# Kernel optimization log

Hardware: AMD Instinct MI355X
Metric: run time of the kernel (lower is better)

## Reference

```python
import jax, jax.numpy as jnp
import numpy as np

B, S, D, H, DFF = 8, 1024, 1024, 16, 4096
DK = D // H
EPS = 1e-6
NEG = -1e9


def setup_inputs() -> dict:
    key = jax.random.key(0)
    ks = jax.random.split(key, 8)
    x = jax.random.normal(ks[0], (B, S, D), dtype=jnp.float32)
    mask = jnp.ones((B, 1, 1, S), dtype=jnp.int32)
    s = 0.02
    wq = jax.random.normal(ks[1], (D, D), jnp.float32) * s
    wk = jax.random.normal(ks[2], (D, D), jnp.float32) * s
    wv = jax.random.normal(ks[3], (D, D), jnp.float32) * s
    wo = jax.random.normal(ks[4], (D, D), jnp.float32) * s
    bq = jnp.zeros((D,), jnp.float32); bk = jnp.zeros((D,), jnp.float32)
    bv = jnp.zeros((D,), jnp.float32); bo = jnp.zeros((D,), jnp.float32)
    w1 = jax.random.normal(ks[5], (D, DFF), jnp.float32) * s
    b1 = jnp.zeros((DFF,), jnp.float32)
    w2 = jax.random.normal(ks[6], (DFF, D), jnp.float32) * s
    b2 = jnp.zeros((D,), jnp.float32)
    g1 = jnp.array(1.0, jnp.float32); be1 = jnp.array(0.0, jnp.float32)
    g2 = jnp.array(1.0, jnp.float32); be2 = jnp.array(0.0, jnp.float32)
    return dict(x=x, mask=mask, wq=wq, bq=bq, wk=wk, bk=bk, wv=wv, bv=bv,
                wo=wo, bo=bo, w1=w1, b1=b1, w2=w2, b2=b2,
                g1=g1, be1=be1, g2=g2, be2=be2)


def layer_norm(x, gamma, beta):
    # repo quirk: unbiased std (ddof=1), scalar gamma/beta, divide by (std+eps)
    mean = jnp.mean(x, axis=-1, keepdims=True)
    std = jnp.std(x, axis=-1, keepdims=True, ddof=1)
    return gamma * (x - mean) / (std + EPS) + beta


def mha(x, mask, wq, bq, wk, bk, wv, bv, wo, bo):
    q = (x @ wq + bq).reshape(B, S, H, DK).transpose(0, 2, 1, 3)  # bhsd
    k = (x @ wk + bk).reshape(B, S, H, DK).transpose(0, 2, 1, 3)
    v = (x @ wv + bv).reshape(B, S, H, DK).transpose(0, 2, 1, 3)
    scores = jnp.einsum('bhqd,bhkd->bhqk', q, k) / jnp.sqrt(jnp.float32(DK))
    scores = jnp.where(mask == 0, NEG, scores)
    attn = jax.nn.softmax(scores, axis=-1)
    out = jnp.einsum('bhqk,bhkd->bhqd', attn, v)
    out = out.transpose(0, 2, 1, 3).reshape(B, S, D)
    return out @ wo + bo


def reference(x, mask, wq, bq, wk, bk, wv, bv, wo, bo, w1, b1, w2, b2, g1, be1, g2, be2):
    # pre-LN residual: x + sublayer(norm(x)); dropout inert at eval
    x = x + mha(layer_norm(x, g1, be1), mask, wq, bq, wk, bk, wv, bv, wo, bo)
    h = layer_norm(x, g2, be2)
    x = x + (jax.nn.relu(h @ w1 + b1) @ w2 + b2)
    return x
```

## Files before the change

### kernel.cpp

```cpp
#include <hip/hip_runtime.h>
#include <math.h>

typedef __bf16 bf16;
typedef float f32x4 __attribute__((ext_vector_type(4)));
typedef bf16 bf16x8 __attribute__((ext_vector_type(8)));
typedef bf16 bf16x4 __attribute__((ext_vector_type(4)));

#define DEV __device__ __forceinline__

constexpr int Ss = 1024, Dd = 1024;
constexpr float EPSf = 1e-6f;
constexpr float SM_SCALE = 0.125f * 1.4426950408889634f;

DEV void gl_lds16(const void* g, void* l) {
  __builtin_amdgcn_global_load_lds(
      (const __attribute__((address_space(1))) void*)g,
      (__attribute__((address_space(3))) void*)l, 16, 0, 0);
}

__global__ __launch_bounds__(256) void transpose6_k(
    const float* __restrict__ i0, const float* __restrict__ i1,
    const float* __restrict__ i2, const float* __restrict__ i3,
    const float* __restrict__ i4, const float* __restrict__ i5,
    bf16* __restrict__ o0, bf16* __restrict__ o1, bf16* __restrict__ o2,
    bf16* __restrict__ o3, bf16* __restrict__ o4, bf16* __restrict__ o5) {
  __shared__ float t[64 * 65];
  const int bi = blockIdx.x;
  const float* in;
  bf16* out;
  int R, C, local, sh;
  if (bi < 1024) {
    const int j = bi >> 8;
    local = bi & 255; R = 1024; C = 1024; sh = 4;
    in = (j == 0) ? i0 : (j == 1) ? i1 : (j == 2) ? i2 : i3;
    out = (j == 0) ? o0 : (j == 1) ? o1 : (j == 2) ? o2 : o3;
  } else if (bi < 2048) {
    local = bi - 1024; R = 1024; C = 4096; sh = 6; in = i4; out = o4;
  } else {
    local = bi - 2048; R = 4096; C = 1024; sh = 4; in = i5; out = o5;
  }
  const int nx = 1 << sh;
  const int bx = local & (nx - 1), by = local >> sh;
  const int tid = threadIdx.x;
  const int tx = tid & 63, ty = tid >> 6;
  const int r0 = by * 64, c0 = bx * 64;
#pragma unroll
  for (int i = 0; i < 16; i++) {
    int r = ty + i * 4;
    t[r * 65 + tx] = in[(size_t)(r0 + r) * C + c0 + tx];
  }
  __syncthreads();
#pragma unroll
  for (int i = 0; i < 16; i++) {
    int r = ty + i * 4;
    out[(size_t)(c0 + r) * R + r0 + tx] = (bf16)t[tx * 65 + r];
  }
}

__global__ __launch_bounds__(256) void ln_kernel(
    const float* __restrict__ in, bf16* __restrict__ out,
    const float* __restrict__ gp, const float* __restrict__ bp) {
  const int row = blockIdx.x;
  const int tid = threadIdx.x;
  float v[4];
  const float* p = in + (size_t)row * Dd + tid * 4;
#pragma unroll
  for (int i = 0; i < 4; i++) v[i] = p[i];
  float s = v[0] + v[1] + v[2] + v[3];
  float s2 = v[0] * v[0] + v[1] * v[1] + v[2] * v[2] + v[3] * v[3];
#pragma unroll
  for (int m = 1; m < 64; m <<= 1) {
    s += __shfl_xor(s, m, 64);
    s2 += __shfl_xor(s2, m, 64);
  }
  __shared__ float ls[4], ls2[4];
  if ((tid & 63) == 0) {
    ls[tid >> 6] = s;
    ls2[tid >> 6] = s2;
  }
  __syncthreads();
  s = ls[0] + ls[1] + ls[2] + ls[3];
  s2 = ls2[0] + ls2[1] + ls2[2] + ls2[3];
  float mean = s * (1.0f / Dd);
  float var = (s2 - (float)Dd * mean * mean) * (1.0f / (Dd - 1));
  var = fmaxf(var, 0.0f);
  float g = gp[0], be = bp[0];
  float rs = g / (sqrtf(var) + EPSf);
  bf16* q = out + (size_t)row * Dd + tid * 4;
#pragma unroll
  for (int i = 0; i < 4; i++) q[i] = (bf16)((v[i] - mean) * rs + be);
}

template <int EPI, int BK>
__global__ __launch_bounds__(256) void gemm_bt(
    const bf16* __restrict__ A, const bf16* __restrict__ Bt,
    const float* __restrict__ bias, const float* __restrict__ bias2,
    const float* __restrict__ bias3, const float* __restrict__ resid,
    bf16* __restrict__ vtb, void* __restrict__ Cout, int M, int N, int K,
    int sa, int sb) {
  __shared__ __attribute__((aligned(16))) char smem[2 * 128 * BK * 2];
  bf16* As = (bf16*)smem;
  bf16* Bs = (bf16*)(smem + 128 * BK * 2);
  constexpr int CPR = BK / 8;
  constexpr int RPJ = 256 / CPR;
  constexpr int NJ = BK / 16;
  const int tid = threadIdx.x;
  const int ln = tid & 63;
  const int wv = tid >> 6;
  const int wm = wv >> 1, wn = wv & 1;
  const int quad = ln >> 4, l16 = ln & 15;
  const int l7 = l16 & 7;
  const int m0 = blockIdx.y * 128, n0 = blockIdx.x * 128;

  f32x4 acc[4][4];
#pragma unroll
  for (int i = 0; i < 4; i++)
#pragma unroll
    for (int j = 0; j < 4; j++) acc[i][j] = {0.f, 0.f, 0.f, 0.f};

  const int sr = tid / CPR;
  const int sc = (tid & (CPR - 1)) ^ (sr & 7);
  const size_t abase = (size_t)(m0 + sr) * sa + sc * 8;
  const size_t bbase = (size_t)(n0 + sr) * sb + sc * 8;

  for (int k0 = 0; k0 < K; k0 += BK) {
#pragma unroll
    for (int j = 0; j < NJ; j++) {
      gl_lds16(A + abase + (size_t)(j * RPJ) * sa + k0,
               (char*)As + j * 4096 + wv * 1024);
      gl_lds16(Bt + bbase + (size_t)(j * RPJ) * sb + k0,
               (char*)Bs + j * 4096 + wv * 1024);
    }
    __syncthreads();
#pragma unroll
    for (int kh = 0; kh < BK / 32; kh++) {
      bf16x8 af[4], bfr[4];
#pragma unroll
      for (int mi = 0; mi < 4; mi++)
        af[mi] = *(const bf16x8*)&As[(wm * 64 + mi * 16 + l16) * BK +
                                     ((kh * 4 + quad) ^ l7) * 8];
#pragma unroll
      for (int ni = 0; ni < 4; ni++)
        bfr[ni] = *(const bf16x8*)&Bs[(wn * 64 + ni * 16 + l16) * BK +
                                      ((kh * 4 + quad) ^ l7) * 8];
#pragma unroll
      for (int mi = 0; mi < 4; mi++)
#pragma unroll
        for (int ni = 0; ni < 4; ni++)
          acc[mi][ni] = __builtin_amdgcn_mfma_f32_16x16x32_bf16(
              af[mi], bfr[ni], acc[mi][ni], 0, 0, 0);
    }
    __syncthreads();
  }

  if constexpr (EPI == 4) {
    if (n0 < 2048) {
#pragma unroll
      for (int mi = 0; mi < 4; mi++) {
        const int m = m0 + wm * 64 + mi * 16 + quad * 4;
#pragma unroll
        for (int ni = 0; ni < 4; ni++) {
          const int n = n0 + wn * 64 + ni * 16 + l16;
          const float bvl = (n < 1024) ? bias[n] : bias2[n - 1024];
#pragma unroll
          for (int r = 0; r < 4; r++)
            ((bf16*)Cout)[(size_t)(m + r) * N + n] =
                (bf16)(acc[mi][ni][r] + bvl);
        }
      }
    } else {
      bf16* T = (bf16*)smem;
#pragma unroll
      for (int mi = 0; mi < 4; mi++) {
        const int ml = wm * 64 + mi * 16 + quad * 4;
        const int c = ml >> 3, hf = (ml >> 2) & 1;
#pragma unroll
        for (int ni = 0; ni < 4; ni++) {
          const int nl = wn * 64 + ni * 16 + l16;
          const float bvl = bias3[(n0 - 2048) + nl];
          bf16x4 tv;
#pragma unroll
          for (int r = 0; r < 4; r++) tv[r] = (bf16)(acc[mi][ni][r] + bvl);
          *(bf16x4*)&T[nl * 128 + ((c ^ (nl & 15)) << 3) + (hf << 2)] = tv;
        }
      }
      __syncthreads();
      const size_t vbase =
          ((size_t)(m0 >> 10) * 1024 + (n0 - 2048)) * Ss + (m0 & 1023);
#pragma unroll
      for (int p = 0; p < 8; p++) {
        const int row = p * 16 + (tid >> 4);
        const int k = tid & 15;
        bf16x8 vv = *(const bf16x8*)&T[row * 128 + ((k ^ (row & 15)) << 3)];
        *(bf16x8*)&vtb[vbase + (size_t)row * Ss + k * 8] = vv;
      }
    }
  } else {
#pragma unroll
    for (int mi = 0; mi < 4; mi++) {
      const int m = m0 + wm * 64 + mi * 16 + quad * 4;
#pragma unroll
      for (int ni = 0; ni < 4; ni++) {
        const int n = n0 + wn * 64 + ni * 16 + l16;
        float bvl = 0.0f;
        if constexpr (EPI != 3) bvl = bias[n];
#pragma unroll
        for (int r = 0; r < 4; r++) {
          float val = acc[mi][ni][r] + bvl;
          const size_t idx = (size_t)(m + r) * N + n;
          if constexpr (EPI == 1) {
            ((float*)Cout)[idx] = val + resid[idx];
          } else if constexpr (EPI == 2) {
            ((bf16*)Cout)[idx] = (bf16)fmaxf(val, 0.0f);
          } else {
            ((float*)Cout)[idx] = val + resid[idx];
          }
        }
      }
    }
  }
}

__global__ __launch_bounds__(256) void attn_k(
    const bf16* __restrict__ qkv, const bf16* __restrict__ vt,
    const int* __restrict__ mask, bf16* __restrict__ ctx) {
  __shared__ __attribute__((aligned(16))) char smem[36864];
  bf16* Qs = (bf16*)smem;
  bf16* Ks = (bf16*)(smem + 16384);
  bf16* Vs = (bf16*)(smem + 24576);
  float* Fm = (float*)(smem + 32768);
  bf16* Ps = Qs;
  const int tid = threadIdx.x;
  const int ln = tid & 63, w = tid >> 6;
  const int quad = ln >> 4, l16 = ln & 15;
  const int l7 = l16 & 7;
  const int bh = blockIdx.y;
  const int b = bh >> 4, h = bh & 15;
  const int q0 = blockIdx.x * 128;
  const int sr = tid >> 3;
  const int sc = (tid & 7) ^ (sr & 7);

  {
#pragma unroll
    for (int j = 0; j < 4; j++) {
      const size_t ga =
          (size_t)(b * Ss + q0 + j * 32 + sr) * 3072 + h * 64 + sc * 8;
      gl_lds16(qkv + ga, (char*)Qs + j * 4096 + w * 1024);
    }
  }
  {
    const int4 mv = *(const int4*)&mask[b * Ss + tid * 4];
    const float ninf = -__builtin_inff();
    Fm[tid * 4 + 0] = mv.x ? 0.0f : ninf;
    Fm[tid * 4 + 1] = mv.y ? 0.0f : ninf;
    Fm[tid * 4 + 2] = mv.z ? 0.0f : ninf;
    Fm[tid * 4 + 3] = mv.w ? 0.0f : ninf;
  }
  __syncthreads();
  bf16x8 aq[2][2];
#pragma unroll
  for (int qi = 0; qi < 2; qi++)
#pragma unroll
    for (int c = 0; c < 2; c++)
      aq[qi][c] = *(const bf16x8*)&Qs[(w * 32 + qi * 16 + l16) * 64 +
                                      ((c * 4 + quad) ^ l7) * 8];

  bf16x8 ONE;
#pragma unroll
  for (int i = 0; i < 8; i++) ONE[i] = (bf16)1.0f;

  f32x4 o[2][4];
#pragma unroll
  for (int qi = 0; qi < 2; qi++)
#pragma unroll
    for (int i = 0; i < 4; i++) o[qi][i] = {0.f, 0.f, 0.f, 0.f};
  f32x4 osum[2] = {{0.f, 0.f, 0.f, 0.f}, {0.f, 0.f, 0.f, 0.f}};

  for (int kk0 = 0; kk0 < Ss; kk0 += 64) {
    {
#pragma unroll
      for (int j = 0; j < 2; j++) {
        const size_t ga = (size_t)(b * Ss + kk0 + j * 32 + sr) * 3072 + 1024 +
                          h * 64 + sc * 8;
        gl_lds16(qkv + ga, (char*)Ks + j * 4096 + w * 1024);
        const size_t gv = (size_t)(bh * 64 + j * 32 + sr) * Ss + kk0 + sc * 8;
        gl_lds16(vt + gv, (char*)Vs + j * 4096 + w * 1024);
      }
    }
    __syncthreads();

    f32x4 st[2][4];
#pragma unroll
    for (int nt = 0; nt < 4; nt++) {
      bf16x8 bk0 = *(const bf16x8*)&Ks[(nt * 16 + l16) * 64 + (quad ^ l7) * 8];
      bf16x8 bk1 =
          *(const bf16x8*)&Ks[(nt * 16 + l16) * 64 + ((4 + quad) ^ l7) * 8];
#pragma unroll
      for (int qi = 0; qi < 2; qi++) {
        f32x4 s = {0.f, 0.f, 0.f, 0.f};
        s = __builtin_amdgcn_mfma_f32_16x16x32_bf16(aq[qi][0], bk0, s, 0, 0, 0);
        s = __builtin_amdgcn_mfma_f32_16x16x32_bf16(aq[qi][1], bk1, s, 0, 0, 0);
        st[qi][nt] = s;
      }
    }
    float fmv[4];
#pragma unroll
    for (int nt = 0; nt < 4; nt++) fmv[nt] = Fm[kk0 + nt * 16 + l16];
#pragma unroll
    for (int qi = 0; qi < 2; qi++)
#pragma unroll
      for (int nt = 0; nt < 4; nt++)
#pragma unroll
        for (int r = 0; r < 4; r++)
          st[qi][nt][r] = exp2f(fmaf(st[qi][nt][r], SM_SCALE, fmv[nt]));
#pragma unroll
    for (int qi = 0; qi < 2; qi++)
#pragma unroll
      for (int nt = 0; nt < 4; nt++) {
        const int ch = nt * 2 + (l16 >> 3);
#pragma unroll
        for (int r = 0; r < 4; r++) {
          const int pr = qi * 16 + quad * 4 + r;
          Ps[w * 2048 + pr * 64 + (ch ^ (pr & 7)) * 8 + l7] =
              (bf16)st[qi][nt][r];
        }
      }
#pragma unroll
    for (int kh = 0; kh < 2; kh++) {
      bf16x8 bv[4];
#pragma unroll
      for (int dt = 0; dt < 4; dt++)
        bv[dt] = *(const bf16x8*)&Vs[(dt * 16 + l16) * 64 +
                                     ((kh * 4 + quad) ^ l7) * 8];
#pragma unroll
      for (int qi = 0; qi < 2; qi++) {
        bf16x8 ap = *(const bf16x8*)&Ps[w * 2048 + (qi * 16 + l16) * 64 +
                                        ((kh * 4 + quad) ^ l7) * 8];
#pragma unroll
        for (int dt = 0; dt < 4; dt++)
          o[qi][dt] =
              __builtin_amdgcn_mfma_f32_16x16x32_bf16(ap, bv[dt], o[qi][dt],
                                                      0, 0, 0);
        osum[qi] =
            __builtin_amdgcn_mfma_f32_16x16x32_bf16(ap, ONE, osum[qi], 0, 0, 0);
      }
    }
    __syncthreads();
  }
#pragma unroll
  for (int qi = 0; qi < 2; qi++) {
    const float inv0 = 1.0f / osum[qi][0], inv1 = 1.0f / osum[qi][1];
    const float inv2 = 1.0f / osum[qi][2], inv3 = 1.0f / osum[qi][3];
#pragma unroll
    for (int dt = 0; dt < 4; dt++) {
      const size_t base =
          (size_t)(b * Ss + q0 + w * 32 + qi * 16 + quad * 4) * Dd + h * 64 +
          dt * 16 + l16;
      ctx[base] = (bf16)(o[qi][dt][0] * inv0);
      ctx[base + Dd] = (bf16)(o[qi][dt][1] * inv1);
      ctx[base + 2 * Dd] = (bf16)(o[qi][dt][2] * inv2);
      ctx[base + 3 * Dd] = (bf16)(o[qi][dt][3] * inv3);
    }
  }
}

extern "C" void kernel_launch(void* const* d_in, const int* in_sizes, int n_in,
                              void* d_out, int out_size, void* d_ws,
                              size_t ws_size, hipStream_t stream) {
  (void)in_sizes; (void)n_in; (void)out_size;
  const float* x = (const float*)d_in[0];
  const int* mask = (const int*)d_in[1];
  const float* wq = (const float*)d_in[2];
  const float* bq = (const float*)d_in[3];
  const float* wk = (const float*)d_in[4];
  const float* bk = (const float*)d_in[5];
  const float* wvw = (const float*)d_in[6];
  const float* bv = (const float*)d_in[7];
  const float* wo = (const float*)d_in[8];
  const float* bo = (const float*)d_in[9];
  const float* w1 = (const float*)d_in[10];
  const float* b1 = (const float*)d_in[11];
  const float* w2 = (const float*)d_in[12];
  const float* b2 = (const float*)d_in[13];
  const float* g1 = (const float*)d_in[14];
  const float* be1 = (const float*)d_in[15];
  const float* g2 = (const float*)d_in[16];
  const float* be2 = (const float*)d_in[17];
  float* out = (float*)d_out;

  char* ws = (char*)d_ws;
  const size_t MB = 1024 * 1024;
  bf16* w1T = (bf16*)(ws + 0 * MB);
  bf16* w2T = (bf16*)(ws + 8 * MB);
  bf16* wqkvT = (bf16*)(ws + 16 * MB);
  bf16* woT = (bf16*)(ws + 22 * MB);
  bf16* lnb = (bf16*)(ws + 24 * MB);
  bf16* qkv = (bf16*)(ws + 40 * MB);
  bf16* vtb = (bf16*)(ws + 88 * MB);
  float* x1 = (float*)(ws + 40 * MB);
  bf16* ctx = lnb;

  dim3 blk(256);
  transpose6_k<<<3072, blk, 0, stream>>>(
      wq, wk, wvw, wo, w1, w2, wqkvT, wqkvT + (size_t)1024 * 1024,
      wqkvT + (size_t)2048 * 1024, woT, w1T, w2T);
  ln_kernel<<<8192, blk, 0, stream>>>(x, lnb, g1, be1);
  gemm_bt<4, 64><<<dim3(24, 64), blk, 0, stream>>>(
      lnb, wqkvT, bq, bk, bv, nullptr, vtb, qkv, 8192, 3072, 1024, 1024, 1024);
  attn_k<<<dim3(8, 128), blk, 0, stream>>>(qkv, vtb, mask, ctx);
  gemm_bt<1, 128><<<dim3(8, 64), blk, 0, stream>>>(
      ctx, woT, bo, nullptr, nullptr, x, nullptr, x1, 8192, 1024, 1024, 1024,
      1024);
  ln_kernel<<<8192, blk, 0, stream>>>(x1, lnb, g2, be2);

  if (ws_size >= 136 * MB) {
    bf16* mid = (bf16*)(ws + 72 * MB);
    gemm_bt<2, 64><<<dim3(32, 64), blk, 0, stream>>>(
        lnb, w1T, b1, nullptr, nullptr, nullptr, nullptr, mid, 8192, 4096,
        1024, 1024, 1024);
    gemm_bt<1, 128><<<dim3(8, 64), blk, 0, stream>>>(
        mid, w2T, b2, nullptr, nullptr, x1, nullptr, out, 8192, 1024, 4096,
        4096, 4096);
  } else {
    bf16* mid = (bf16*)(ws + 72 * MB);
    gemm_bt<2, 64><<<dim3(16, 64), blk, 0, stream>>>(
        lnb, w1T, b1, nullptr, nullptr, nullptr, nullptr, mid, 8192, 2048,
        1024, 1024, 1024);
    gemm_bt<1, 128><<<dim3(8, 64), blk, 0, stream>>>(
        mid, w2T, b2, nullptr, nullptr, x1, nullptr, out, 8192, 1024, 2048,
        2048, 4096);
    gemm_bt<2, 64><<<dim3(16, 64), blk, 0, stream>>>(
        lnb, w1T + (size_t)2048 * 1024, b1 + 2048, nullptr, nullptr, nullptr,
        nullptr, mid, 8192, 2048, 1024, 1024, 1024);
    gemm_bt<3, 128><<<dim3(8, 64), blk, 0, stream>>>(
        mid, w2T + 2048, nullptr, nullptr, nullptr, out, nullptr, out, 8192,
        1024, 2048, 2048, 4096);
  }
}
```

Measured before the change: 494.0 us.

## Rewrite attention with 32x32 MFMA, register-resident P and mask-skip fast path

Restructures the attention kernel to use 32x32x16 MFMA computing S^T, so probabilities stay in registers and are repacked with cvt_pk and permlane32_swap instead of round-tripping through LDS. Row sums come from VALU adds rather than an extra MFMA against a ones vector. A per-tile mask flag skips the mask add when a key tile is fully unmasked, and the output is staged through LDS for coalesced 16-byte stores. The grid is also swapped so head-batch varies fastest, and setprio hints are added. This removes LDS traffic and redundant MFMA work, but softmax still has no max subtraction and the kernel relies on gfx950-specific instructions.

```diff
diff --git a/kernel.cpp b/kernel.cpp
--- a/kernel.cpp
+++ b/kernel.cpp
@@ -3,8 +3,11 @@
 
 typedef __bf16 bf16;
 typedef float f32x4 __attribute__((ext_vector_type(4)));
+typedef float f32x16 __attribute__((ext_vector_type(16)));
 typedef bf16 bf16x8 __attribute__((ext_vector_type(8)));
 typedef bf16 bf16x4 __attribute__((ext_vector_type(4)));
+typedef unsigned int u32;
+typedef unsigned int u32x2 __attribute__((ext_vector_type(2)));
 
 #define DEV __device__ __forceinline__
 
@@ -16,6 +19,12 @@
   __builtin_amdgcn_global_load_lds(
       (const __attribute__((address_space(1))) void*)g,
       (__attribute__((address_space(3))) void*)l, 16, 0, 0);
+}
+
+DEV u32 cvtpk(float lo, float hi) {
+  u32 r;
+  asm("v_cvt_pk_bf16_f32 %0, %1, %2" : "=v"(r) : "v"(lo), "v"(hi));
+  return r;
 }
 
 __global__ __launch_bounds__(256) void transpose6_k(
@@ -225,21 +234,22 @@
     const bf16* __restrict__ qkv, const bf16* __restrict__ vt,
     const int* __restrict__ mask, bf16* __restrict__ ctx) {
   __shared__ __attribute__((aligned(16))) char smem[36864];
+  __shared__ int Ft[16];
   bf16* Qs = (bf16*)smem;
   bf16* Ks = (bf16*)(smem + 16384);
   bf16* Vs = (bf16*)(smem + 24576);
   float* Fm = (float*)(smem + 32768);
-  bf16* Ps = Qs;
   const int tid = threadIdx.x;
-  const int ln = tid & 63, w = tid >> 6;
-  const int quad = ln >> 4, l16 = ln & 15;
-  const int l7 = l16 & 7;
-  const int bh = blockIdx.y;
+  const int l = tid & 63, w = tid >> 6;
+  const int lq = l & 31, lh = l >> 5;
+  const int lq7 = lq & 7;
+  const int bh = blockIdx.x;
   const int b = bh >> 4, h = bh & 15;
-  const int q0 = blockIdx.x * 128;
+  const int q0 = blockIdx.y * 128;
   const int sr = tid >> 3;
   const int sc = (tid & 7) ^ (sr & 7);
 
+  if (tid < 16) Ft[tid] = 0;
   {
 #pragma unroll
     for (int j = 0; j < 4; j++) {
@@ -248,6 +258,14 @@
       gl_lds16(qkv + ga, (char*)Qs + j * 4096 + w * 1024);
     }
   }
+  __syncthreads();
+
+  bf16x8 qf[4];
+#pragma unroll
+  for (int s = 0; s < 4; s++)
+    qf[s] =
+        *(const bf16x8*)&Qs[(w * 32 + lq) * 64 + (((s * 2 + lh) ^ lq7) * 8)];
+
   {
     const int4 mv = *(const int4*)&mask[b * Ss + tid * 4];
     const float ninf = -__builtin_inff();
@@ -255,26 +273,15 @@
     Fm[tid * 4 + 1] = mv.y ? 0.0f : ninf;
     Fm[tid * 4 + 2] = mv.z ? 0.0f : ninf;
     Fm[tid * 4 + 3] = mv.w ? 0.0f : ninf;
-  }
-  __syncthreads();
-  bf16x8 aq[2][2];
-#pragma unroll
-  for (int qi = 0; qi < 2; qi++)
-#pragma unroll
-    for (int c = 0; c < 2; c++)
-      aq[qi][c] = *(const bf16x8*)&Qs[(w * 32 + qi * 16 + l16) * 64 +
-                                      ((c * 4 + quad) ^ l7) * 8];
-
-  bf16x8 ONE;
-#pragma unroll
-  for (int i = 0; i < 8; i++) ONE[i] = (bf16)1.0f;
-
-  f32x4 o[2][4];
-#pragma unroll
-  for (int qi = 0; qi < 2; qi++)
-#pragma unroll
-    for (int i = 0; i < 4; i++) o[qi][i] = {0.f, 0.f, 0.f, 0.f};
-  f32x4 osum[2] = {{0.f, 0.f, 0.f, 0.f}, {0.f, 0.f, 0.f, 0.f}};
+    if (!(mv.x && mv.y && mv.z && mv.w)) atomicOr(&Ft[tid >> 4], 1);
+  }
+
+  f32x16 oacc[2];
+#pragma unroll
+  for (int d = 0; d < 2; d++)
+#pragma unroll
+    for (int r = 0; r < 16; r++) oacc[d][r] = 0.0f;
+  float rsum = 0.0f;
 
   for (int kk0 = 0; kk0 < Ss; kk0 += 64) {
     {
@@ -289,78 +296,110 @@
     }
     __syncthreads();
 
-    f32x4 st[2][4];
-#pragma unroll
-    for (int nt = 0; nt < 4; nt++) {
-      bf16x8 bk0 = *(const bf16x8*)&Ks[(nt * 16 + l16) * 64 + (quad ^ l7) * 8];
-      bf16x8 bk1 =
-          *(const bf16x8*)&Ks[(nt * 16 + l16) * 64 + ((4 + quad) ^ l7) * 8];
-#pragma unroll
-      for (int qi = 0; qi < 2; qi++) {
-        f32x4 s = {0.f, 0.f, 0.f, 0.f};
-        s = __builtin_amdgcn_mfma_f32_16x16x32_bf16(aq[qi][0], bk0, s, 0, 0, 0);
-        s = __builtin_amdgcn_mfma_f32_16x16x32_bf16(aq[qi][1], bk1, s, 0, 0, 0);
-        st[qi][nt] = s;
-      }
-    }
-    float fmv[4];
-#pragma unroll
-    for (int nt = 0; nt < 4; nt++) fmv[nt] = Fm[kk0 + nt * 16 + l16];
-#pragma unroll
-    for (int qi = 0; qi < 2; qi++)
-#pragma unroll
-      for (int nt = 0; nt < 4; nt++)
-#pragma unroll
-        for (int r = 0; r < 4; r++)
-          st[qi][nt][r] = exp2f(fmaf(st[qi][nt][r], SM_SCALE, fmv[nt]));
-#pragma unroll
-    for (int qi = 0; qi < 2; qi++)
-#pragma unroll
-      for (int nt = 0; nt < 4; nt++) {
-        const int ch = nt * 2 + (l16 >> 3);
-#pragma unroll
-        for (int r = 0; r < 4; r++) {
-          const int pr = qi * 16 + quad * 4 + r;
-          Ps[w * 2048 + pr * 64 + (ch ^ (pr & 7)) * 8 + l7] =
-              (bf16)st[qi][nt][r];
+    f32x16 sacc[2];
+#pragma unroll
+    for (int kb = 0; kb < 2; kb++)
+#pragma unroll
+      for (int r = 0; r < 16; r++) sacc[kb][r] = 0.0f;
+
+    __builtin_amdgcn_s_setprio(1);
+#pragma unroll
+    for (int kb = 0; kb < 2; kb++)
+#pragma unroll
+      for (int s = 0; s < 4; s++) {
+        const bf16x8 kf = *(const bf16x8*)&Ks[(kb * 32 + lq) * 64 +
+                                              (((s * 2 + lh) ^ lq7) * 8)];
+        sacc[kb] = __builtin_amdgcn_mfma_f32_32x32x16_bf16(kf, qf[s],
+                                                           sacc[kb], 0, 0, 0);
+      }
+    __builtin_amdgcn_s_setprio(0);
+
+    if (__builtin_amdgcn_readfirstlane(Ft[kk0 >> 6])) {
+#pragma unroll
+      for (int kb = 0; kb < 2; kb++)
+#pragma unroll
+        for (int g = 0; g < 4; g++) {
+          const f32x4 mv = *(const f32x4*)&Fm[kk0 + kb * 32 + 4 * lh + 8 * g];
+#pragma unroll
+          for (int j = 0; j < 4; j++)
+            sacc[kb][g * 4 + j] = __builtin_amdgcn_exp2f(
+                fmaf(sacc[kb][g * 4 + j], SM_SCALE, mv[j]));
         }
-      }
-#pragma unroll
-    for (int kh = 0; kh < 2; kh++) {
-      bf16x8 bv[4];
-#pragma unroll
-      for (int dt = 0; dt < 4; dt++)
-        bv[dt] = *(const bf16x8*)&Vs[(dt * 16 + l16) * 64 +
-                                     ((kh * 4 + quad) ^ l7) * 8];
-#pragma unroll
-      for (int qi = 0; qi < 2; qi++) {
-        bf16x8 ap = *(const bf16x8*)&Ps[w * 2048 + (qi * 16 + l16) * 64 +
-                                        ((kh * 4 + quad) ^ l7) * 8];
-#pragma unroll
-        for (int dt = 0; dt < 4; dt++)
-          o[qi][dt] =
-              __builtin_amdgcn_mfma_f32_16x16x32_bf16(ap, bv[dt], o[qi][dt],
-                                                      0, 0, 0);
-        osum[qi] =
-            __builtin_amdgcn_mfma_f32_16x16x32_bf16(ap, ONE, osum[qi], 0, 0, 0);
-      }
-    }
+    } else {
+#pragma unroll
+      for (int kb = 0; kb < 2; kb++)
+#pragma unroll
+        for (int r = 0; r < 16; r++)
+          sacc[kb][r] = __builtin_amdgcn_exp2f(sacc[kb][r] * SM_SCALE);
+    }
+#pragma unroll
+    for (int kb = 0; kb < 2; kb++) {
+      const float t0 = (sacc[kb][0] + sacc[kb][1]) + (sacc[kb][2] + sacc[kb][3]);
+      const float t1 = (sacc[kb][4] + sacc[kb][5]) + (sacc[kb][6] + sacc[kb][7]);
+      const float t2 =
+          (sacc[kb][8] + sacc[kb][9]) + (sacc[kb][10] + sacc[kb][11]);
+      const float t3 =
+          (sacc[kb][12] + sacc[kb][13]) + (sacc[kb][14] + sacc[kb][15]);
+      rsum += ((t0 + t1) + (t2 + t3));
+    }
+
+    __builtin_amdgcn_s_setprio(1);
+#pragma unroll
+    for (int t = 0; t < 4; t++) {
+      const int kb = t >> 1, rb = (t & 1) * 8;
+      u32 pa = cvtpk(sacc[kb][rb + 0], sacc[kb][rb + 1]);
+      u32 pbv = cvtpk(sacc[kb][rb + 2], sacc[kb][rb + 3]);
+      u32 pc = cvtpk(sacc[kb][rb + 4], sacc[kb][rb + 5]);
+      u32 pd = cvtpk(sacc[kb][rb + 6], sacc[kb][rb + 7]);
+      asm("v_permlane32_swap_b32 %0, %1" : "+v"(pa), "+v"(pc));
+      asm("v_permlane32_swap_b32 %0, %1" : "+v"(pbv), "+v"(pd));
+      union {
+        u32 u[4];
+        bf16x8 v;
+      } pk;
+      pk.u[0] = pa;
+      pk.u[1] = pbv;
+      pk.u[2] = pc;
+      pk.u[3] = pd;
+      const int vsw = ((t * 2 + lh) ^ lq7) * 8;
+      const bf16x8 vf0 = *(const bf16x8*)&Vs[lq * 64 + vsw];
+      const bf16x8 vf1 = *(const bf16x8*)&Vs[(32 + lq) * 64 + vsw];
+      oacc[0] =
+          __builtin_amdgcn_mfma_f32_32x32x16_bf16(vf0, pk.v, oacc[0], 0, 0, 0);
+      oacc[1] =
+          __builtin_amdgcn_mfma_f32_32x32x16_bf16(vf1, pk.v, oacc[1], 0, 0, 0);
+    }
+    __builtin_amdgcn_s_setprio(0);
     __syncthreads();
   }
-#pragma unroll
-  for (int qi = 0; qi < 2; qi++) {
-    const float inv0 = 1.0f / osum[qi][0], inv1 = 1.0f / osum[qi][1];
-    const float inv2 = 1.0f / osum[qi][2], inv3 = 1.0f / osum[qi][3];
-#pragma unroll
-    for (int dt = 0; dt < 4; dt++) {
-      const size_t base =
-          (size_t)(b * Ss + q0 + w * 32 + qi * 16 + quad * 4) * Dd + h * 64 +
-          dt * 16 + l16;
-      ctx[base] = (bf16)(o[qi][dt][0] * inv0);
-      ctx[base + Dd] = (bf16)(o[qi][dt][1] * inv1);
-      ctx[base + 2 * Dd] = (bf16)(o[qi][dt][2] * inv2);
-      ctx[base + 3 * Dd] = (bf16)(o[qi][dt][3] * inv3);
-    }
+
+  float xs = rsum, ys = rsum;
+  asm("v_permlane32_swap_b32 %0, %1" : "+v"(xs), "+v"(ys));
+  const float inv = 1.0f / (xs + ys);
+
+  bf16* Tb = (bf16*)(smem + w * 4608);
+#pragma unroll
+  for (int dblk = 0; dblk < 2; dblk++)
+#pragma unroll
+    for (int g = 0; g < 4; g++) {
+      const u32 lo =
+          cvtpk(oacc[dblk][g * 4 + 0] * inv, oacc[dblk][g * 4 + 1] * inv);
+      const u32 hi =
+          cvtpk(oacc[dblk][g * 4 + 2] * inv, oacc[dblk][g * 4 + 3] * inv);
+      u32x2 pr2;
+      pr2[0] = lo;
+      pr2[1] = hi;
+      const int dbase = dblk * 32 + 8 * g + 4 * lh;
+      *(u32x2*)&Tb[lq * 72 + dbase] = pr2;
+    }
+  __syncthreads();
+#pragma unroll
+  for (int p = 0; p < 4; p++) {
+    const int row = p * 8 + (l >> 3);
+    const int ch = l & 7;
+    const bf16x8 vv = *(const bf16x8*)&Tb[row * 72 + ch * 8];
+    *(bf16x8*)&ctx[(size_t)(b * Ss + q0 + w * 32 + row) * Dd + h * 64 +
+                   ch * 8] = vv;
   }
 }
 
@@ -407,7 +446,7 @@
   ln_kernel<<<8192, blk, 0, stream>>>(x, lnb, g1, be1);
   gemm_bt<4, 64><<<dim3(24, 64), blk, 0, stream>>>(
       lnb, wqkvT, bq, bk, bv, nullptr, vtb, qkv, 8192, 3072, 1024, 1024, 1024);
-  attn_k<<<dim3(8, 128), blk, 0, stream>>>(qkv, vtb, mask, ctx);
+  attn_k<<<dim3(128, 8), blk, 0, stream>>>(qkv, vtb, mask, ctx);
   gemm_bt<1, 128><<<dim3(8, 64), blk, 0, stream>>>(
       ctx, woT, bo, nullptr, nullptr, x, nullptr, x1, 8192, 1024, 1024, 1024,
       1024);
```

Result: faster. 470.0 us (-4.9%).
